# Kernel tuning notes

Measured on AMD Instinct MI355X. Metric: run time of the kernel, lower is better.

## Reference

```python
import jax, jax.numpy as jnp
import numpy as np

N_HEAD = 8
LN_EPS = 1e-5


def _ln(x, g, b):
    m = jnp.mean(x, axis=-1, keepdims=True)
    v = jnp.mean((x - m) ** 2, axis=-1, keepdims=True)
    return (x - m) * jax.lax.rsqrt(v + LN_EPS) * g + b


def setup_inputs() -> dict:
    B, S, IN, D, F, OUT, L = 4, 2048, 3, 512, 2048, 20, 6
    key = jax.random.key(0)
    ks = jax.random.split(key, 22)
    sc = 0.02
    return {
        'src': jax.random.normal(ks[0], (B, S, IN), jnp.float32),
        'W_in': jax.random.normal(ks[1], (IN, D), jnp.float32) * sc,
        'b_in': jnp.zeros((D,), jnp.float32),
        'Wq': jax.random.normal(ks[2], (L, D, D), jnp.float32) * sc,
        'bq': jnp.zeros((L, D), jnp.float32),
        'Wk': jax.random.normal(ks[3], (L, D, D), jnp.float32) * sc,
        'bk': jnp.zeros((L, D), jnp.float32),
        'Wv': jax.random.normal(ks[4], (L, D, D), jnp.float32) * sc,
        'bv': jnp.zeros((L, D), jnp.float32),
        'Wo': jax.random.normal(ks[5], (L, D, D), jnp.float32) * sc,
        'bo': jnp.zeros((L, D), jnp.float32),
        'ln1_g': jnp.ones((L, D), jnp.float32),
        'ln1_b': jnp.zeros((L, D), jnp.float32),
        'W1': jax.random.normal(ks[6], (L, D, F), jnp.float32) * sc,
        'b1': jnp.zeros((L, F), jnp.float32),
        'W2': jax.random.normal(ks[7], (L, F, D), jnp.float32) * sc,
        'b2': jnp.zeros((L, D), jnp.float32),
        'ln2_g': jnp.ones((L, D), jnp.float32),
        'ln2_b': jnp.zeros((L, D), jnp.float32),
        'W_out': jax.random.normal(ks[8], (D, OUT), jnp.float32) * sc,
        'b_out': jnp.zeros((OUT,), jnp.float32),
    }


def reference(src, W_in, b_in, Wq, bq, Wk, bk, Wv, bv, Wo, bo, ln1_g, ln1_b,
              W1, b1, W2, b2, ln2_g, ln2_b, W_out, b_out):
    x = src @ W_in + b_in            # [B, S, D]
    B, S, D = x.shape
    dh = D // N_HEAD
    scale = 1.0 / np.sqrt(dh).astype(np.float32)

    def layer(x, p):
        wq, biq, wk, bik, wv, biv, wo, bio, g1, be1, w1, bi1, w2, bi2, g2, be2 = p
        q = (x @ wq + biq).reshape(B, S, N_HEAD, dh)
        k = (x @ wk + bik).reshape(B, S, N_HEAD, dh)
        v = (x @ wv + biv).reshape(B, S, N_HEAD, dh)
        # flex_attention with score_mod=None == plain scaled dot-product attention
        scores = jnp.einsum('bqhd,bkhd->bhqk', q, k) * scale
        a = jax.nn.softmax(scores, axis=-1)
        o = jnp.einsum('bhqk,bkhd->bqhd', a, v).reshape(B, S, D)
        attn = o @ wo + bio
        h = _ln(x + attn, g1, be1)                       # post-norm (norm_first=False)
        ff = jax.nn.relu(h @ w1 + bi1) @ w2 + bi2
        h = _ln(h + ff, g2, be2)
        return h, None

    x, _ = jax.lax.scan(layer, x, (Wq, bq, Wk, bk, Wv, bv, Wo, bo,
                                   ln1_g, ln1_b, W1, b1, W2, b2, ln2_g, ln2_b))
    return x @ W_out + b_out         # [B, S, OUT]
```

## Files before the change

kernel.cpp:

```cpp
#include <hip/hip_runtime.h>

typedef unsigned short u16;
typedef unsigned int u32;
typedef __bf16 bf16x8 __attribute__((ext_vector_type(8)));
typedef float f32x4 __attribute__((ext_vector_type(4)));
typedef float f32x16 __attribute__((ext_vector_type(16)));

__device__ __forceinline__ u16 f2bf(float f) {
    union { float f; u32 u; } v; v.f = f;
    u32 r = v.u + 0x7FFFu + ((v.u >> 16) & 1u);
    return (u16)(r >> 16);
}

__device__ __forceinline__ u16 bfu(float x) {
    __bf16 b = (__bf16)x;
    union { __bf16 b; u16 u; } c; c.b = b; return c.u;
}

__device__ __forceinline__ void pl32swap(u32& a, u32& b) {
    asm volatile("v_permlane32_swap_b32 %0, %1" : "+v"(a), "+v"(b));
}

__device__ __forceinline__ void gload16(const u16* g, u16* l) {
    __builtin_amdgcn_global_load_lds((const __attribute__((address_space(1))) void*)g,
                                     (__attribute__((address_space(3))) void*)l, 16, 0, 0);
}

__global__ void wtrans(const float* __restrict__ W, u16* __restrict__ Wt,
                       int K, int N, int rowOff, int dstLd, long long dstStride)
{
    __shared__ float tile[32][33];
    const int l = blockIdx.z;
    const float* Wl = W + (size_t)l * K * N;
    u16* Wtl = Wt + (size_t)l * dstStride;
    const int tx = threadIdx.x, ty = threadIdx.y;
    const int x = blockIdx.x * 32 + tx;
    const int y0 = blockIdx.y * 32;
#pragma unroll
    for (int j = 0; j < 32; j += 8) tile[ty + j][tx] = Wl[(size_t)(y0 + ty + j) * N + x];
    __syncthreads();
    const int n0 = blockIdx.x * 32;
    const int k = y0 + tx;
#pragma unroll
    for (int j = 0; j < 32; j += 8)
        Wtl[(size_t)(rowOff + n0 + ty + j) * dstLd + k] = f2bf(tile[tx][ty + j]);
}

__global__ __launch_bounds__(256) void input_proj(const float* __restrict__ src,
    const float* __restrict__ Wi, const float* __restrict__ bi,
    float* __restrict__ xf, u16* __restrict__ xb)
{
    int idx = blockIdx.x * 256 + threadIdx.x;
    int m = idx >> 9, n = idx & 511;
    float v = bi[n] + src[m * 3] * Wi[n] + src[m * 3 + 1] * Wi[512 + n] + src[m * 3 + 2] * Wi[1024 + n];
    xf[idx] = v;
    xb[idx] = f2bf(v);
}

template<int EPI>
__global__ __launch_bounds__(256) void gemm_bt(
    const u16* __restrict__ A, const u16* __restrict__ Bt,
    const float* __restrict__ bias,
    float* __restrict__ Cf, u16* __restrict__ Cb,
    u16* __restrict__ Qo, u16* __restrict__ Ko, u16* __restrict__ Vo,
    const float* __restrict__ bq, const float* __restrict__ bk, const float* __restrict__ bv,
    int M, int N, int K)
{
    __shared__ u16 As[128 * 64];
    __shared__ u16 Bs[128 * 64];
    const int tid = threadIdx.x;
    const int lane = tid & 63, wid = tid >> 6;
    const int row0 = blockIdx.y * 128, col0 = blockIdx.x * 128;
    const int wr = (wid >> 1) * 64, wc = (wid & 1) * 64;
    const int cc = lane & 15, qg = lane >> 4;
    const int sr = tid >> 3, sg = tid & 7;
    f32x4 acc[4][4] = {};
    for (int k0 = 0; k0 < K; k0 += 64) {
        __syncthreads();
#pragma unroll
        for (int j = 0; j < 4; j++) {
            int r = j * 32 + sr;
            int gsw = (sg ^ (r & 7)) * 8;
            gload16(A + (size_t)(row0 + r) * K + k0 + gsw, &As[(j * 256 + tid) * 8]);
        }
#pragma unroll
        for (int j = 0; j < 4; j++) {
            int r = j * 32 + sr;
            int gsw = (sg ^ (r & 7)) * 8;
            gload16(Bt + (size_t)(col0 + r) * K + k0 + gsw, &Bs[(j * 256 + tid) * 8]);
        }
        __syncthreads();
        bf16x8 af[4][2], bfr[4][2];
#pragma unroll
        for (int i = 0; i < 4; i++) {
            int r = wr + i * 16 + cc;
#pragma unroll
            for (int kk = 0; kk < 2; kk++)
                af[i][kk] = *(const bf16x8*)&As[r * 64 + ((kk * 4 + qg) ^ (r & 7)) * 8];
        }
#pragma unroll
        for (int i = 0; i < 4; i++) {
            int r = wc + i * 16 + cc;
#pragma unroll
            for (int kk = 0; kk < 2; kk++)
                bfr[i][kk] = *(const bf16x8*)&Bs[r * 64 + ((kk * 4 + qg) ^ (r & 7)) * 8];
        }
#pragma unroll
        for (int mi = 0; mi < 4; mi++)
#pragma unroll
            for (int ni = 0; ni < 4; ni++) {
                acc[mi][ni] = __builtin_amdgcn_mfma_f32_16x16x32_bf16(af[mi][0], bfr[ni][0], acc[mi][ni], 0, 0, 0);
                acc[mi][ni] = __builtin_amdgcn_mfma_f32_16x16x32_bf16(af[mi][1], bfr[ni][1], acc[mi][ni], 0, 0, 0);
            }
    }
    const int q4 = qg * 4;
    if (EPI == 2) {
#pragma unroll
        for (int mi = 0; mi < 4; mi++) {
            int grow = row0 + wr + mi * 16 + q4;
            int btok = grow >> 11, srem = grow & 2047;
#pragma unroll
            for (int ni = 0; ni < 4; ni++) {
                int gcol = col0 + wc + ni * 16 + cc;
                int sec = gcol >> 9, f = gcol & 511;
                int hh = f >> 6, dd = f & 63;
                if (sec == 0) {
                    float bb = bq[f];
                    size_t base = (((size_t)btok * 8 + hh) * 2048 + srem) * 64 + dd;
#pragma unroll
                    for (int i = 0; i < 4; i++) Qo[base + (size_t)i * 64] = f2bf((acc[mi][ni][i] + bb) * 0.18033688f);
                } else if (sec == 1) {
                    float bb = bk[f];
                    size_t base = (((size_t)btok * 8 + hh) * 2048 + srem) * 64 + dd;
#pragma unroll
                    for (int i = 0; i < 4; i++) Ko[base + (size_t)i * 64] = f2bf(acc[mi][ni][i] + bb);
                } else {
                    float bb = bv[f];
                    size_t base = (((size_t)btok * 8 + hh) * 64 + dd) * 2048 + srem;
#pragma unroll
                    for (int i = 0; i < 4; i++) Vo[base + i] = f2bf(acc[mi][ni][i] + bb);
                }
            }
        }
    } else {
#pragma unroll
        for (int mi = 0; mi < 4; mi++) {
            int grow = row0 + wr + mi * 16 + q4;
#pragma unroll
            for (int ni = 0; ni < 4; ni++) {
                int gcol = col0 + wc + ni * 16 + cc;
                float bb = bias[gcol];
#pragma unroll
                for (int i = 0; i < 4; i++) {
                    float v = acc[mi][ni][i] + bb;
                    if (EPI == 0) Cf[(size_t)(grow + i) * N + gcol] = v;
                    else          Cb[(size_t)(grow + i) * N + gcol] = f2bf(v > 0.f ? v : 0.f);
                }
            }
        }
    }
}

__global__ __launch_bounds__(256) void gemm64_db(
    const u16* __restrict__ A, const u16* __restrict__ Bt,
    const float* __restrict__ bias, const float* __restrict__ Rf,
    float* __restrict__ Cf, int M, int N, int K)
{
    __shared__ u16 As[2][64 * 64];
    __shared__ u16 Bs[2][64 * 64];
    const int tid = threadIdx.x;
    const int lane = tid & 63, wid = tid >> 6;
    const int row0 = blockIdx.y * 64, col0 = blockIdx.x * 64;
    const int wr = (wid >> 1) * 32, wc = (wid & 1) * 32;
    const int cc = lane & 15, qg = lane >> 4;
    const int r0 = tid >> 3, g8 = (tid & 7);
    const int gsw0 = (g8 ^ (r0 & 7)) * 8;
    const int r1 = r0 + 32;
    const int gsw1 = (g8 ^ (r1 & 7)) * 8;
    f32x4 acc[2][2] = {};
    gload16(A + (size_t)(row0 + r0) * K + gsw0, &As[0][tid * 8]);
    gload16(A + (size_t)(row0 + r1) * K + gsw1, &As[0][(tid + 256) * 8]);
    gload16(Bt + (size_t)(col0 + r0) * K + gsw0, &Bs[0][tid * 8]);
    gload16(Bt + (size_t)(col0 + r1) * K + gsw1, &Bs[0][(tid + 256) * 8]);
    int cur = 0;
    for (int k0 = 0; k0 < K; k0 += 64) {
        asm volatile("s_waitcnt vmcnt(0)" ::: "memory");
        __syncthreads();
        if (k0 + 64 < K) {
            int kn = k0 + 64, nb = cur ^ 1;
            gload16(A + (size_t)(row0 + r0) * K + kn + gsw0, &As[nb][tid * 8]);
            gload16(A + (size_t)(row0 + r1) * K + kn + gsw1, &As[nb][(tid + 256) * 8]);
            gload16(Bt + (size_t)(col0 + r0) * K + kn + gsw0, &Bs[nb][tid * 8]);
            gload16(Bt + (size_t)(col0 + r1) * K + kn + gsw1, &Bs[nb][(tid + 256) * 8]);
        }
        bf16x8 af[2][2], bfr[2][2];
#pragma unroll
        for (int i = 0; i < 2; i++) {
            int r = wr + i * 16 + cc;
#pragma unroll
            for (int kk = 0; kk < 2; kk++)
                af[i][kk] = *(const bf16x8*)&As[cur][r * 64 + ((kk * 4 + qg) ^ (r & 7)) * 8];
        }
#pragma unroll
        for (int i = 0; i < 2; i++) {
            int r = wc + i * 16 + cc;
#pragma unroll
            for (int kk = 0; kk < 2; kk++)
                bfr[i][kk] = *(const bf16x8*)&Bs[cur][r * 64 + ((kk * 4 + qg) ^ (r & 7)) * 8];
        }
        __builtin_amdgcn_s_setprio(1);
#pragma unroll
        for (int mi = 0; mi < 2; mi++)
#pragma unroll
            for (int ni = 0; ni < 2; ni++) {
                acc[mi][ni] = __builtin_amdgcn_mfma_f32_16x16x32_bf16(af[mi][0], bfr[ni][0], acc[mi][ni], 0, 0, 0);
                acc[mi][ni] = __builtin_amdgcn_mfma_f32_16x16x32_bf16(af[mi][1], bfr[ni][1], acc[mi][ni], 0, 0, 0);
            }
        __builtin_amdgcn_s_setprio(0);
        cur ^= 1;
    }
    const int q4 = qg * 4;
#pragma unroll
    for (int mi = 0; mi < 2; mi++) {
        int grow = row0 + wr + mi * 16 + q4;
#pragma unroll
        for (int ni = 0; ni < 2; ni++) {
            int gcol = col0 + wc + ni * 16 + cc;
            float bb = bias[gcol];
#pragma unroll
            for (int i = 0; i < 4; i++) {
                size_t idx = (size_t)(grow + i) * N + gcol;
                Cf[idx] = acc[mi][ni][i] + bb + Rf[idx];
            }
        }
    }
}

__global__ __launch_bounds__(256) void flash_attn(
    const u16* __restrict__ Qb, const u16* __restrict__ Kb, const u16* __restrict__ Vt,
    u16* __restrict__ Ob)
{
    __shared__ u16 Ks[2][4096];
    __shared__ u16 Vs[2][4096];
    const int tid = threadIdx.x, lane = tid & 63, w = tid >> 6;
    const int l31 = lane & 31, h = lane >> 5;
    const int bh = blockIdx.x, qt = blockIdx.y;
    const u16* Kg = Kb + (size_t)bh * (2048 * 64);
    const u16* Vg = Vt + (size_t)bh * (64 * 2048);

    bf16x8 qf[4];
    {
        const u16* Qrow = Qb + ((size_t)bh * 2048 + (size_t)qt * 128 + w * 32 + l31) * 64;
#pragma unroll
        for (int f = 0; f < 4; f++) qf[f] = *(const bf16x8*)(Qrow + f * 16 + h * 8);
    }
    f32x16 os0{}, os1{};
    float lsum = 0.f;

    const int r8 = lane >> 3;
    const int cswz = ((lane & 7) ^ r8) * 8;
#pragma unroll
    for (int cc = 0; cc < 2; cc++) {
        int c = w * 2 + cc;
        gload16(Kg + (size_t)(c * 8 + r8) * 64 + cswz, &Ks[0][c * 512]);
        gload16(Vg + (size_t)(c * 8 + r8) * 2048 + cswz, &Vs[0][c * 512]);
    }
    const int swz = (l31 & 7) << 3;

    for (int kt = 0; kt < 32; kt++) {
        const int cur = kt & 1;
        asm volatile("s_waitcnt vmcnt(0)" ::: "memory");
        __syncthreads();
        if (kt < 31) {
#pragma unroll
            for (int cc = 0; cc < 2; cc++) {
                int c = w * 2 + cc;
                gload16(Kg + (size_t)(kt + 1) * 4096 + (size_t)(c * 8 + r8) * 64 + cswz, &Ks[cur ^ 1][c * 512]);
                gload16(Vg + (size_t)(c * 8 + r8) * 2048 + (size_t)(kt + 1) * 64 + cswz, &Vs[cur ^ 1][c * 512]);
            }
        }
        f32x16 p0{}, p1{};
        {
            const u16* kb = &Ks[cur][0];
            __builtin_amdgcn_s_setprio(1);
#pragma unroll
            for (int f = 0; f < 4; f++) {
                int colu = (f * 16 + h * 8) ^ swz;
                bf16x8 ka0 = *(const bf16x8*)(kb + l31 * 64 + colu);
                bf16x8 ka1 = *(const bf16x8*)(kb + (32 + l31) * 64 + colu);
                p0 = __builtin_amdgcn_mfma_f32_32x32x16_bf16(ka0, qf[f], p0, 0, 0, 0);
                p1 = __builtin_amdgcn_mfma_f32_32x32x16_bf16(ka1, qf[f], p1, 0, 0, 0);
            }
            __builtin_amdgcn_s_setprio(0);
        }
        float ss[4] = {};
#pragma unroll
        for (int r = 0; r < 16; r++) { float e = __builtin_amdgcn_exp2f(p0[r]); p0[r] = e; ss[r & 3] += e; }
#pragma unroll
        for (int r = 0; r < 16; r++) { float e = __builtin_amdgcn_exp2f(p1[r]); p1[r] = e; ss[r & 3] += e; }
        lsum += (ss[0] + ss[1]) + (ss[2] + ss[3]);
        const u16* vb = &Vs[cur][0];
#pragma unroll
        for (int t = 0; t < 2; t++) {
            u32 pk[8];
#pragma unroll
            for (int j = 0; j < 8; j++) {
                float a = t ? p1[2 * j] : p0[2 * j];
                float b = t ? p1[2 * j + 1] : p0[2 * j + 1];
                pk[j] = (u32)bfu(a) | ((u32)bfu(b) << 16);
            }
            u32 x0 = pk[0], y0 = pk[2]; pl32swap(x0, y0);
            u32 x1 = pk[1], y1 = pk[3]; pl32swap(x1, y1);
            u32 x2 = pk[4], y2 = pk[6]; pl32swap(x2, y2);
            u32 x3 = pk[5], y3 = pk[7]; pl32swap(x3, y3);
            union { u32 u[4]; bf16x8 v; } fA, fB;
            fA.u[0] = x0; fA.u[1] = x1; fA.u[2] = y0; fA.u[3] = y1;
            fB.u[0] = x2; fB.u[1] = x3; fB.u[2] = y2; fB.u[3] = y3;
            __builtin_amdgcn_s_setprio(1);
#pragma unroll
            for (int f = 0; f < 2; f++) {
                bf16x8 pa = f ? fB.v : fA.v;
                int colu = (t * 32 + f * 16 + h * 8) ^ swz;
                bf16x8 v0 = *(const bf16x8*)(vb + l31 * 64 + colu);
                bf16x8 v1 = *(const bf16x8*)(vb + (32 + l31) * 64 + colu);
                os0 = __builtin_amdgcn_mfma_f32_32x32x16_bf16(pa, v0, os0, 0, 0, 0);
                os1 = __builtin_amdgcn_mfma_f32_32x32x16_bf16(pa, v1, os1, 0, 0, 0);
            }
            __builtin_amdgcn_s_setprio(0);
        }
    }
    lsum += __shfl_xor(lsum, 32);
    float rl = 1.f / lsum;
    const int hatt = bh & 7, b_ = bh >> 3;
#pragma unroll
    for (int r = 0; r < 16; r++) {
        int qrow = (r & 3) + 8 * (r >> 2) + 4 * h;
        float rlq = __shfl(rl, qrow);
        int tok = qt * 128 + w * 32 + qrow;
        u16* po = Ob + ((size_t)b_ * 2048 + tok) * 512 + hatt * 64;
        po[l31] = bfu(os0[r] * rlq);
        po[32 + l31] = bfu(os1[r] * rlq);
    }
}

__global__ __launch_bounds__(256) void ln_one(
    const float* __restrict__ Y,
    const float* __restrict__ g, const float* __restrict__ bta,
    float* __restrict__ Of, u16* __restrict__ Ob)
{
    const int lane = threadIdx.x & 63;
    const int row = blockIdx.x * 4 + (threadIdx.x >> 6);
    const size_t base = (size_t)row * 512 + lane * 8;
    float4 y0 = *(const float4*)(Y + base);
    float4 y1 = *(const float4*)(Y + base + 4);
    float t[8] = {y0.x, y0.y, y0.z, y0.w, y1.x, y1.y, y1.z, y1.w};
    float s = 0.f, s2 = 0.f;
#pragma unroll
    for (int j = 0; j < 8; j++) { s += t[j]; s2 += t[j] * t[j]; }
#pragma unroll
    for (int off = 1; off < 64; off <<= 1) { s += __shfl_xor(s, off); s2 += __shfl_xor(s2, off); }
    float mean = s * (1.f / 512.f);
    float var = s2 * (1.f / 512.f) - mean * mean;
    float rs = rsqrtf(var + 1e-5f);
    float4 g0 = *(const float4*)(g + lane * 8);
    float4 g1 = *(const float4*)(g + lane * 8 + 4);
    float4 b0 = *(const float4*)(bta + lane * 8);
    float4 b1 = *(const float4*)(bta + lane * 8 + 4);
    float gg[8] = {g0.x, g0.y, g0.z, g0.w, g1.x, g1.y, g1.z, g1.w};
    float bb[8] = {b0.x, b0.y, b0.z, b0.w, b1.x, b1.y, b1.z, b1.w};
    float o[8];
#pragma unroll
    for (int j = 0; j < 8; j++) o[j] = (t[j] - mean) * rs * gg[j] + bb[j];
    *(float4*)(Of + base) = make_float4(o[0], o[1], o[2], o[3]);
    *(float4*)(Of + base + 4) = make_float4(o[4], o[5], o[6], o[7]);
    u32 p0 = (u32)f2bf(o[0]) | ((u32)f2bf(o[1]) << 16);
    u32 p1 = (u32)f2bf(o[2]) | ((u32)f2bf(o[3]) << 16);
    u32 p2 = (u32)f2bf(o[4]) | ((u32)f2bf(o[5]) << 16);
    u32 p3 = (u32)f2bf(o[6]) | ((u32)f2bf(o[7]) << 16);
    *(uint4*)(Ob + base) = make_uint4(p0, p1, p2, p3);
}

__global__ __launch_bounds__(320) void out_proj(const float* __restrict__ x,
    const float* __restrict__ W, const float* __restrict__ b, float* __restrict__ out)
{
    int t = blockIdx.x * 320 + threadIdx.x;
    int m = t / 20, o = t - m * 20;
    const float* xr = x + (size_t)m * 512;
    float a0 = b[o], a1 = 0.f, a2 = 0.f, a3 = 0.f;
#pragma unroll 4
    for (int k = 0; k < 512; k += 4) {
        a0 = fmaf(xr[k],     W[k * 20 + o],       a0);
        a1 = fmaf(xr[k + 1], W[(k + 1) * 20 + o], a1);
        a2 = fmaf(xr[k + 2], W[(k + 2) * 20 + o], a2);
        a3 = fmaf(xr[k + 3], W[(k + 3) * 20 + o], a3);
    }
    out[(size_t)m * 20 + o] = (a0 + a1) + (a2 + a3);
}

extern "C" void kernel_launch(void* const* d_in, const int* in_sizes, int n_in,
                              void* d_out, int out_size, void* d_ws, size_t ws_size,
                              hipStream_t stream)
{
    const float* src  = (const float*)d_in[0];
    const float* W_in = (const float*)d_in[1];
    const float* b_in = (const float*)d_in[2];
    const float* Wq   = (const float*)d_in[3];
    const float* bq   = (const float*)d_in[4];
    const float* Wk   = (const float*)d_in[5];
    const float* bk   = (const float*)d_in[6];
    const float* Wv   = (const float*)d_in[7];
    const float* bv   = (const float*)d_in[8];
    const float* Wo   = (const float*)d_in[9];
    const float* bo   = (const float*)d_in[10];
    const float* ln1g = (const float*)d_in[11];
    const float* ln1b = (const float*)d_in[12];
    const float* W1   = (const float*)d_in[13];
    const float* b1   = (const float*)d_in[14];
    const float* W2   = (const float*)d_in[15];
    const float* b2   = (const float*)d_in[16];
    const float* ln2g = (const float*)d_in[17];
    const float* ln2b = (const float*)d_in[18];
    const float* Wout = (const float*)d_in[19];
    const float* bout = (const float*)d_in[20];

    char* ws = (char*)d_ws;
    size_t off = 0;
    auto take = [&](size_t bytes) -> void* {
        off = (off + 255) & ~(size_t)255;
        void* p = ws + off;
        off += bytes;
        return p;
    };
    const size_t TOK = 8192, D = 512;
    u16*   qkvt = (u16*)take(6ull * 1536 * 512 * 2);
    u16*   wot  = (u16*)take(6ull * 512 * 512 * 2);
    u16*   w1t  = (u16*)take(6ull * 2048 * 512 * 2);
    u16*   w2t  = (u16*)take(6ull * 512 * 2048 * 2);
    float* xf   = (float*)take(TOK * D * 4);
    u16*   xb   = (u16*)take(TOK * D * 2);
    u16*   sh4  = (u16*)take(4ull * TOK * D * 2);
    float* scr  = (float*)take(TOK * D * 4);
    float* h1f  = (float*)take(TOK * D * 4);
    u16*   h1b  = (u16*)take(TOK * D * 2);
    if (off > ws_size) return;

    u16* qb  = sh4;
    u16* kb_ = sh4 + TOK * D;
    u16* vtb = sh4 + 2 * TOK * D;
    u16* ob  = sh4 + 3 * TOK * D;
    u16* ffb = sh4;

    dim3 tb(32, 8);
    wtrans<<<dim3(16, 16, 6), tb, 0, stream>>>(Wq, qkvt, 512, 512, 0,    512, 1536ll * 512);
    wtrans<<<dim3(16, 16, 6), tb, 0, stream>>>(Wk, qkvt, 512, 512, 512,  512, 1536ll * 512);
    wtrans<<<dim3(16, 16, 6), tb, 0, stream>>>(Wv, qkvt, 512, 512, 1024, 512, 1536ll * 512);
    wtrans<<<dim3(16, 16, 6), tb, 0, stream>>>(Wo, wot,  512, 512, 0,    512, 512ll * 512);
    wtrans<<<dim3(64, 16, 6), tb, 0, stream>>>(W1, w1t,  512, 2048, 0,   512, 2048ll * 512);
    wtrans<<<dim3(16, 64, 6), tb, 0, stream>>>(W2, w2t,  2048, 512, 0,  2048, 512ll * 2048);

    input_proj<<<16384, 256, 0, stream>>>(src, W_in, b_in, xf, xb);

    for (int l = 0; l < 6; l++) {
        const u16* qkvt_l = qkvt + (size_t)l * 1536 * 512;
        const u16* wot_l  = wot  + (size_t)l * 512 * 512;
        const u16* w1t_l  = w1t  + (size_t)l * 2048 * 512;
        const u16* w2t_l  = w2t  + (size_t)l * 512 * 2048;

        gemm_bt<2><<<dim3(12, 64), 256, 0, stream>>>(xb, qkvt_l, nullptr,
            nullptr, nullptr, qb, kb_, vtb,
            bq + l * 512, bk + l * 512, bv + l * 512, 8192, 1536, 512);

        flash_attn<<<dim3(32, 16), 256, 0, stream>>>(qb, kb_, vtb, ob);

        gemm64_db<<<dim3(8, 128), 256, 0, stream>>>(ob, wot_l, bo + l * 512,
            xf, scr, 8192, 512, 512);

        ln_one<<<2048, 256, 0, stream>>>(scr, ln1g + l * 512, ln1b + l * 512, h1f, h1b);

        gemm_bt<1><<<dim3(16, 64), 256, 0, stream>>>(h1b, w1t_l, b1 + l * 2048,
            nullptr, ffb, nullptr, nullptr, nullptr, nullptr, nullptr, nullptr,
            8192, 2048, 512);

        gemm64_db<<<dim3(8, 128), 256, 0, stream>>>(ffb, w2t_l, b2 + l * 512,
            h1f, scr, 8192, 512, 2048);

        ln_one<<<2048, 256, 0, stream>>>(scr, ln2g + l * 512, ln2b + l * 512, xf, xb);
    }

    out_proj<<<512, 320, 0, stream>>>(xf, Wout, bout, (float*)d_out);
}
```

Baseline: 1.100 ms.

## Replace 128x128 GEMM with 256x256 tile, 4-stage LDS pipeline for QKV and FFN1

Result: slower. 1.204 ms (+9.4%).

```diff
diff --git a/kernel.cpp b/kernel.cpp
--- a/kernel.cpp
+++ b/kernel.cpp
@@ -57,71 +57,86 @@
     xb[idx] = f2bf(v);
 }
 
+__device__ __forceinline__ void stage_tile256(const u16* __restrict__ G, int ld, int row0,
+                                              int k0, u16* lds, int tid)
+{
+#pragma unroll
+    for (int j = 0; j < 2; j++) {
+        int s = tid + j * 512;
+        int R = s >> 3;
+        int u = (s & 7) ^ (R & 7);
+        int r = 2 * R + (u >> 2);
+        int gc = u & 3;
+        gload16(G + (size_t)(row0 + r) * ld + k0 + gc * 8, lds + s * 8);
+    }
+}
+
 template<int EPI>
-__global__ __launch_bounds__(256) void gemm_bt(
+__global__ __launch_bounds__(512, 2) void gemm256(
     const u16* __restrict__ A, const u16* __restrict__ Bt,
-    const float* __restrict__ bias,
-    float* __restrict__ Cf, u16* __restrict__ Cb,
+    const float* __restrict__ bias, u16* __restrict__ Cb,
     u16* __restrict__ Qo, u16* __restrict__ Ko, u16* __restrict__ Vo,
     const float* __restrict__ bq, const float* __restrict__ bk, const float* __restrict__ bv,
     int M, int N, int K)
 {
-    __shared__ u16 As[128 * 64];
-    __shared__ u16 Bs[128 * 64];
-    const int tid = threadIdx.x;
-    const int lane = tid & 63, wid = tid >> 6;
-    const int row0 = blockIdx.y * 128, col0 = blockIdx.x * 128;
-    const int wr = (wid >> 1) * 64, wc = (wid & 1) * 64;
+    __shared__ u16 As[4][8192];
+    __shared__ u16 Bs[4][8192];
+    const int tid = threadIdx.x, lane = tid & 63, wid = tid >> 6;
+    const int wm = wid >> 2, wn = wid & 3;
+    const int row0 = blockIdx.y * 256, col0 = blockIdx.x * 256;
     const int cc = lane & 15, qg = lane >> 4;
-    const int sr = tid >> 3, sg = tid & 7;
-    f32x4 acc[4][4] = {};
-    for (int k0 = 0; k0 < K; k0 += 64) {
-        __syncthreads();
-#pragma unroll
-        for (int j = 0; j < 4; j++) {
-            int r = j * 32 + sr;
-            int gsw = (sg ^ (r & 7)) * 8;
-            gload16(A + (size_t)(row0 + r) * K + k0 + gsw, &As[(j * 256 + tid) * 8]);
-        }
-#pragma unroll
-        for (int j = 0; j < 4; j++) {
-            int r = j * 32 + sr;
-            int gsw = (sg ^ (r & 7)) * 8;
-            gload16(Bt + (size_t)(col0 + r) * K + k0 + gsw, &Bs[(j * 256 + tid) * 8]);
-        }
-        __syncthreads();
-        bf16x8 af[4][2], bfr[4][2];
+    f32x4 acc[8][4] = {};
+
+    stage_tile256(A, K, row0, 0, As[0], tid);  stage_tile256(Bt, K, col0, 0, Bs[0], tid);
+    stage_tile256(A, K, row0, 32, As[1], tid); stage_tile256(Bt, K, col0, 32, Bs[1], tid);
+    stage_tile256(A, K, row0, 64, As[2], tid); stage_tile256(Bt, K, col0, 64, Bs[2], tid);
+
+    for (int t = 0; t < 16; ++t) {
+        if (t <= 13)      asm volatile("s_waitcnt vmcnt(8)" ::: "memory");
+        else if (t == 14) asm volatile("s_waitcnt vmcnt(4)" ::: "memory");
+        else              asm volatile("s_waitcnt vmcnt(0)" ::: "memory");
+        __builtin_amdgcn_s_barrier();
+        __builtin_amdgcn_sched_barrier(0);
+        if (t + 3 < 16) {
+            int sl = (t + 3) & 3, k0 = (t + 3) * 32;
+            stage_tile256(A, K, row0, k0, As[sl], tid);
+            stage_tile256(Bt, K, col0, k0, Bs[sl], tid);
+        }
+        const int cs = t & 3;
+        bf16x8 af[8], bfr[4];
+#pragma unroll
+        for (int i = 0; i < 8; i++) {
+            int r = wm * 128 + i * 16 + cc;
+            int R = r >> 1;
+            int g = (((r & 1) << 2) | qg) ^ (R & 7);
+            af[i] = *(const bf16x8*)&As[cs][R * 64 + g * 8];
+        }
 #pragma unroll
         for (int i = 0; i < 4; i++) {
-            int r = wr + i * 16 + cc;
-#pragma unroll
-            for (int kk = 0; kk < 2; kk++)
-                af[i][kk] = *(const bf16x8*)&As[r * 64 + ((kk * 4 + qg) ^ (r & 7)) * 8];
-        }
-#pragma unroll
-        for (int i = 0; i < 4; i++) {
-            int r = wc + i * 16 + cc;
-#pragma unroll
-            for (int kk = 0; kk < 2; kk++)
-                bfr[i][kk] = *(const bf16x8*)&Bs[r * 64 + ((kk * 4 + qg) ^ (r & 7)) * 8];
-        }
-#pragma unroll
-        for (int mi = 0; mi < 4; mi++)
-#pragma unroll
-            for (int ni = 0; ni < 4; ni++) {
-                acc[mi][ni] = __builtin_amdgcn_mfma_f32_16x16x32_bf16(af[mi][0], bfr[ni][0], acc[mi][ni], 0, 0, 0);
-                acc[mi][ni] = __builtin_amdgcn_mfma_f32_16x16x32_bf16(af[mi][1], bfr[ni][1], acc[mi][ni], 0, 0, 0);
-            }
+            int r = wn * 64 + i * 16 + cc;
+            int R = r >> 1;
+            int g = (((r & 1) << 2) | qg) ^ (R & 7);
+            bfr[i] = *(const bf16x8*)&Bs[cs][R * 64 + g * 8];
+        }
+        asm volatile("s_waitcnt lgkmcnt(0)" ::: "memory");
+        __builtin_amdgcn_sched_barrier(0);
+        __builtin_amdgcn_s_setprio(1);
+#pragma unroll
+        for (int mi = 0; mi < 8; mi++)
+#pragma unroll
+            for (int ni = 0; ni < 4; ni++)
+                acc[mi][ni] = __builtin_amdgcn_mfma_f32_16x16x32_bf16(af[mi], bfr[ni], acc[mi][ni], 0, 0, 0);
+        __builtin_amdgcn_s_setprio(0);
     }
     const int q4 = qg * 4;
     if (EPI == 2) {
 #pragma unroll
-        for (int mi = 0; mi < 4; mi++) {
-            int grow = row0 + wr + mi * 16 + q4;
+        for (int mi = 0; mi < 8; mi++) {
+            int grow = row0 + wm * 128 + mi * 16 + q4;
             int btok = grow >> 11, srem = grow & 2047;
 #pragma unroll
             for (int ni = 0; ni < 4; ni++) {
-                int gcol = col0 + wc + ni * 16 + cc;
+                int gcol = col0 + wn * 64 + ni * 16 + cc;
                 int sec = gcol >> 9, f = gcol & 511;
                 int hh = f >> 6, dd = f & 63;
                 if (sec == 0) {
@@ -144,17 +159,16 @@
         }
     } else {
 #pragma unroll
-        for (int mi = 0; mi < 4; mi++) {
-            int grow = row0 + wr + mi * 16 + q4;
+        for (int mi = 0; mi < 8; mi++) {
+            int grow = row0 + wm * 128 + mi * 16 + q4;
 #pragma unroll
             for (int ni = 0; ni < 4; ni++) {
-                int gcol = col0 + wc + ni * 16 + cc;
+                int gcol = col0 + wn * 64 + ni * 16 + cc;
                 float bb = bias[gcol];
 #pragma unroll
                 for (int i = 0; i < 4; i++) {
                     float v = acc[mi][ni][i] + bb;
-                    if (EPI == 0) Cf[(size_t)(grow + i) * N + gcol] = v;
-                    else          Cb[(size_t)(grow + i) * N + gcol] = f2bf(v > 0.f ? v : 0.f);
+                    Cb[(size_t)(grow + i) * N + gcol] = f2bf(v > 0.f ? v : 0.f);
                 }
             }
         }
@@ -466,8 +480,8 @@
         const u16* w1t_l  = w1t  + (size_t)l * 2048 * 512;
         const u16* w2t_l  = w2t  + (size_t)l * 512 * 2048;
 
-        gemm_bt<2><<<dim3(12, 64), 256, 0, stream>>>(xb, qkvt_l, nullptr,
-            nullptr, nullptr, qb, kb_, vtb,
+        gemm256<2><<<dim3(6, 32), 512, 0, stream>>>(xb, qkvt_l, nullptr,
+            nullptr, qb, kb_, vtb,
             bq + l * 512, bk + l * 512, bv + l * 512, 8192, 1536, 512);
 
         flash_attn<<<dim3(32, 16), 256, 0, stream>>>(qb, kb_, vtb, ob);
@@ -477,9 +491,8 @@
 
         ln_one<<<2048, 256, 0, stream>>>(scr, ln1g + l * 512, ln1b + l * 512, h1f, h1b);
 
-        gemm_bt<1><<<dim3(16, 64), 256, 0, stream>>>(h1b, w1t_l, b1 + l * 2048,
-            nullptr, ffb, nullptr, nullptr, nullptr, nullptr, nullptr, nullptr,
-            8192, 2048, 512);
+        gemm256<1><<<dim3(8, 32), 512, 0, stream>>>(h1b, w1t_l, b1 + l * 2048,
+            ffb, nullptr, nullptr, nullptr, nullptr, nullptr, nullptr, 8192, 2048, 512);
 
         gemm64_db<<<dim3(8, 128), 256, 0, stream>>>(ffb, w2t_l, b2 + l * 512,
             h1f, scr, 8192, 512, 2048);
```
